# Kernel tuning notes

Measured on AMD Instinct MI355X. Metric: run time of the kernel, lower is better.

## Reference

```python
import jax, jax.numpy as jnp
import numpy as np

NUM_HEADS = 8
DIM_HEAD = 48
SCALE = DIM_HEAD ** -0.5


def setup_inputs() -> dict:
    key = jax.random.key(0)
    k1, k2, k3 = jax.random.split(key, 3)
    B, N, D = 4, 2048, 384
    inner = NUM_HEADS * DIM_HEAD  # 384
    x = jax.random.normal(k1, (B, N, D), dtype=jnp.float32)
    # store weights in [in, out] layout (equivalent to torch Linear W.T)
    Wqkv = jax.random.normal(k2, (D, 3 * inner), dtype=jnp.float32) * (D ** -0.5)
    Wproj = jax.random.normal(k3, (inner, D), dtype=jnp.float32) * (inner ** -0.5)
    bproj = jnp.zeros((D,), dtype=jnp.float32)
    return {"x": x, "Wqkv": Wqkv, "Wproj": Wproj, "bproj": bproj}


def reference(x, Wqkv, Wproj, bproj):
    B, N, D = x.shape
    h, dh = NUM_HEADS, DIM_HEAD
    C = h * dh
    # fused QKV projection (qkv_bias=False)
    qkv = (x @ Wqkv).reshape(B, N, 3, h, dh)
    q = qkv[:, :, 0].transpose(0, 2, 1, 3)  # [B, h, N, dh]
    k = qkv[:, :, 1].transpose(0, 2, 1, 3)
    v = qkv[:, :, 2].transpose(0, 2, 1, 3)
    # naive attention: materialize [B, h, N, N] scores
    sim = jnp.einsum("bhqd,bhkd->bhqk", q, k) * SCALE
    attn = jax.nn.softmax(sim, axis=-1)
    out = jnp.einsum("bhqk,bhkd->bhqd", attn, v)  # [B, h, N, dh]
    out = out.transpose(0, 2, 1, 3).reshape(B, N, C)
    return out @ Wproj + bproj
```

## Files before the change

kernel.cpp:

```cpp
#include <hip/hip_runtime.h>
#include <hip/hip_bf16.h>


typedef _Float16 f16x8 __attribute__((ext_vector_type(8)));
typedef _Float16 f16x4 __attribute__((ext_vector_type(4)));
typedef _Float16 f16x2 __attribute__((ext_vector_type(2)));
typedef float    f32x4 __attribute__((ext_vector_type(4)));
typedef float    f32x16 __attribute__((ext_vector_type(16)));

#define QSCL 0.20822035963448658f

static __device__ __forceinline__ f16x2 cvt_pk_f16(float a, float b) {
    return __builtin_bit_cast(f16x2, __builtin_amdgcn_cvt_pkrtz(a, b));
}

__global__ __launch_bounds__(256) void prep(const float4* __restrict__ x,
                                            const float* __restrict__ wq,
                                            const float* __restrict__ wp,
                                            f16x4* __restrict__ xh4,
                                            _Float16* __restrict__ wqt,
                                            _Float16* __restrict__ wpt)
{
    __shared__ _Float16 t[64][65];
    const int blk = blockIdx.x, tid = threadIdx.x;
    if (blk < 144) {
        const float* src; _Float16* dst; int Nn, k0, n0;
        if (blk < 108) {
            src = wq; dst = wqt; Nn = 1152;
            k0 = (blk % 6) * 64; n0 = (blk / 6) * 64;
        } else {
            const int b2 = blk - 108;
            src = wp; dst = wpt; Nn = 384;
            k0 = (b2 % 6) * 64; n0 = (b2 / 6) * 64;
        }
        #pragma unroll
        for (int i = 0; i < 16; i++) {
            const int id = tid + i * 256;
            const int k = id >> 6, n = id & 63;
            t[k][n] = (_Float16)src[(size_t)(k0 + k) * Nn + n0 + n];
        }
        __syncthreads();
        #pragma unroll
        for (int i = 0; i < 16; i++) {
            const int id = tid + i * 256;
            const int n = id >> 6, k = id & 63;
            dst[(size_t)(n0 + n) * 384 + k0 + k] = t[k][n];
        }
    } else {
        const int base = (blk - 144) * 3072;
        #pragma unroll
        for (int r = 0; r < 12; r++) {
            const int j = base + r * 256 + tid;
            const float4 tt = x[j];
            f16x4 hh;
            hh[0] = (_Float16)tt.x; hh[1] = (_Float16)tt.y;
            hh[2] = (_Float16)tt.z; hh[3] = (_Float16)tt.w;
            xh4[j] = hh;
        }
    }
}

union QkvSmem {
    struct { _Float16 As[2][128][40]; _Float16 Bs[2][128][40]; } g;
    _Float16 Ts[128][136];
    _Float16 Ts2[128][136];
};

__global__ __launch_bounds__(256) void qkv_f16(const _Float16* __restrict__ A,
                                               const _Float16* __restrict__ Bt,
                                               _Float16* __restrict__ qh,
                                               _Float16* __restrict__ kh,
                                               _Float16* __restrict__ vt)
{
    __shared__ QkvSmem sm;
    const int tid = threadIdx.x;
    const int w = tid >> 6, lane = tid & 63, cl = lane & 15, quad = lane >> 4;
    const int bm = blockIdx.x, bn = blockIdx.y;

    f32x4 acc[2][8];
    const f32x4 z4 = {0.f, 0.f, 0.f, 0.f};
    #pragma unroll
    for (int mi = 0; mi < 2; mi++)
        #pragma unroll
        for (int t = 0; t < 8; t++) acc[mi][t] = z4;

    const int ar = tid >> 2, ac = (tid & 3) * 8;
    const _Float16* Ag = A  + (size_t)(bm * 128 + ar) * 384 + ac;
    const _Float16* Bg = Bt + (size_t)(bn * 128 + ar) * 384 + ac;

    f16x8 pa[2], pb[2];
    #pragma unroll
    for (int j = 0; j < 2; j++) {
        pa[j] = *(const f16x8*)(Ag + (size_t)(64 * j) * 384);
        pb[j] = *(const f16x8*)(Bg + (size_t)(64 * j) * 384);
    }
    #pragma unroll
    for (int j = 0; j < 2; j++) {
        *(f16x8*)&sm.g.As[0][ar + 64 * j][ac] = pa[j];
        *(f16x8*)&sm.g.Bs[0][ar + 64 * j][ac] = pb[j];
    }
    #pragma unroll
    for (int j = 0; j < 2; j++) {
        pa[j] = *(const f16x8*)(Ag + (size_t)(64 * j) * 384 + 32);
        pb[j] = *(const f16x8*)(Bg + (size_t)(64 * j) * 384 + 32);
    }
    __syncthreads();

    for (int it = 0; it < 12; ++it) {
        if (it < 11) {
            #pragma unroll
            for (int j = 0; j < 2; j++) {
                *(f16x8*)&sm.g.As[(it + 1) & 1][ar + 64 * j][ac] = pa[j];
                *(f16x8*)&sm.g.Bs[(it + 1) & 1][ar + 64 * j][ac] = pb[j];
            }
            if (it < 10) {
                const int off = (it + 2) * 32;
                #pragma unroll
                for (int j = 0; j < 2; j++) {
                    pa[j] = *(const f16x8*)(Ag + (size_t)(64 * j) * 384 + off);
                    pb[j] = *(const f16x8*)(Bg + (size_t)(64 * j) * 384 + off);
                }
            }
        }
        f16x8 bf[8];
        #pragma unroll
        for (int t = 0; t < 8; t++)
            bf[t] = *(const f16x8*)&sm.g.Bs[it & 1][t * 16 + cl][quad * 8];
        #pragma unroll
        for (int mi = 0; mi < 2; mi++) {
            const f16x8 af = *(const f16x8*)&sm.g.As[it & 1][w * 32 + mi * 16 + cl][quad * 8];
            #pragma unroll
            for (int t = 0; t < 8; t++)
                acc[mi][t] = __builtin_amdgcn_mfma_f32_16x16x32_f16(af, bf[t], acc[mi][t], 0, 0, 0);
        }
        __syncthreads();
    }

    const int s = (bn * 128) / 384;
    const int b  = (bm * 128) >> 11;
    const int n0 = (bm * 128) & 2047;
    if (s == 2) {
        const int qp = ((quad & 1) << 1) | (quad >> 1);
        #pragma unroll
        for (int t = 0; t < 8; t++)
            #pragma unroll
            for (int mi = 0; mi < 2; mi++)
                #pragma unroll
                for (int r = 0; r < 4; r++)
                    sm.Ts[t * 16 + cl][w * 32 + mi * 16 + qp * 4 + r] =
                        (_Float16)acc[mi][t][r];
        __syncthreads();
        const int colbase = bn * 128 - 768;
        #pragma unroll
        for (int i = 0; i < 8; i++) {
            const int c = i * 256 + tid;
            const int col = c >> 4, nc = c & 15;
            const int gcol = colbase + col;
            const int head = gcol / 48, d = gcol - head * 48;
            const int bh = b * 8 + head;
            *(f16x8*)&vt[(size_t)(bh * 48 + d) * 2048 + n0 + nc * 8] =
                *(const f16x8*)&sm.Ts[col][nc * 8];
        }
    } else {
        const float scl = (s == 0) ? QSCL : 1.0f;
        #pragma unroll
        for (int t = 0; t < 8; t++)
            #pragma unroll
            for (int mi = 0; mi < 2; mi++)
                #pragma unroll
                for (int r = 0; r < 4; r++)
                    sm.Ts2[w * 32 + mi * 16 + quad * 4 + r][t * 16 + cl] =
                        (_Float16)(acc[mi][t][r] * scl);
        __syncthreads();
        _Float16* dst = (s == 0) ? qh : kh;
        const int colbase = bn * 128 - s * 384;
        #pragma unroll
        for (int i = 0; i < 8; i++) {
            const int c = i * 256 + tid;
            const int row = c >> 4, ch = c & 15;
            const int gcol = colbase + ch * 8;
            const int head = gcol / 48, d = gcol - head * 48;
            const int bh = b * 8 + head;
            *(f16x8*)&dst[(size_t)(bh * 2048 + n0 + row) * 48 + d] =
                *(const f16x8*)&sm.Ts2[row][ch * 8];
        }
    }
}

#define KS_S 56
#define VS_S 72

union AttnSmem {
    struct {
        _Float16 Ks[2][2][64][KS_S];
        _Float16 Vts[2][2][64][VS_S];
    } a;
    struct {
        float    Of[128][52];
        float    lv[128];
        _Float16 Ot[128][58];
    } e;
};

__global__ __launch_bounds__(512) void attn_f16(const _Float16* __restrict__ qh,
                                                const _Float16* __restrict__ kh,
                                                const _Float16* __restrict__ vt,
                                                _Float16* __restrict__ ab)
{
    __shared__ AttnSmem sm;
    const int tid = threadIdx.x;
    const int w = tid >> 6, lane = tid & 63, ln = lane & 31, h = lane >> 5;
    const int g = w >> 2, wg = w & 3;
    const int tid2 = tid & 255;
    const int bh = blockIdx.x, qt = blockIdx.y;

    for (int i = tid; i < 2 * 2 * 16 * VS_S; i += 512) {
        const int gi = i / (2 * 16 * VS_S);
        const int j  = i - gi * (2 * 16 * VS_S);
        const int bi = j / (16 * VS_S);
        const int j2 = j - bi * (16 * VS_S);
        const int r = 48 + j2 / VS_S, c = j2 % VS_S;
        sm.a.Vts[gi][bi][r][c] = (r == 48) ? (_Float16)1.0f : (_Float16)0.0f;
    }

    f16x8 qf[3];
    {
        const _Float16* qp = qh + (size_t)(bh * 2048 + qt * 128 + wg * 32 + ln) * 48 + 8 * h;
        qf[0] = *(const f16x8*)qp;
        qf[1] = *(const f16x8*)(qp + 16);
        qf[2] = *(const f16x8*)(qp + 32);
    }

    f32x16 o0, o1;
    #pragma unroll
    for (int r = 0; r < 16; r++) { o0[r] = 0.f; o1[r] = 0.f; }

    const _Float16* kbase = kh + (size_t)bh * 2048 * 48 + (size_t)g * 1024 * 48;
    const _Float16* vbase = vt + (size_t)bh * 48 * 2048 + g * 1024;

    const int kr0 = tid2 / 6,        kc0 = (tid2 % 6) * 8;
    const int kid1 = tid2 + 256;
    const int kr1 = kid1 / 6,        kc1 = (kid1 % 6) * 8;
    const int vr0 = tid2 >> 3,       vc0 = (tid2 & 7) * 8;
    const int vr1 = vr0 + 32;
    const _Float16* ks0 = kbase + (size_t)kr0 * 48 + kc0;
    const _Float16* ks1 = kbase + (size_t)kr1 * 48 + kc1;
    const _Float16* vs0 = vbase + (size_t)vr0 * 2048 + vc0;
    const _Float16* vs1 = vbase + (size_t)vr1 * 2048 + vc0;

    f16x8 rk0 = *(const f16x8*)ks0;
    f16x8 rv0 = *(const f16x8*)vs0;
    f16x8 rk1, rv1;
    if (tid2 < 128) { rk1 = *(const f16x8*)ks1; rv1 = *(const f16x8*)vs1; }

    {
        _Float16 (*Ksb)[KS_S] = sm.a.Ks[g][0];
        _Float16 (*Vtb)[VS_S] = sm.a.Vts[g][0];
        *(f16x8*)&Ksb[kr0][kc0] = rk0;
        *(f16x8*)&Vtb[vr0][vc0] = rv0;
        if (tid2 < 128) {
            *(f16x8*)&Ksb[kr1][kc1] = rk1;
            *(f16x8*)&Vtb[vr1][vc0] = rv1;
        }
        rk0 = *(const f16x8*)(ks0 + (size_t)64 * 48);
        rv0 = *(const f16x8*)(vs0 + 64);
        if (tid2 < 128) {
            rk1 = *(const f16x8*)(ks1 + (size_t)64 * 48);
            rv1 = *(const f16x8*)(vs1 + 64);
        }
        __syncthreads();
    }

    for (int t = 0; t < 16; ++t) {
        if (t < 15) {
            _Float16 (*Ksn)[KS_S] = sm.a.Ks[g][(t + 1) & 1];
            _Float16 (*Vtn)[VS_S] = sm.a.Vts[g][(t + 1) & 1];
            *(f16x8*)&Ksn[kr0][kc0] = rk0;
            *(f16x8*)&Vtn[vr0][vc0] = rv0;
            if (tid2 < 128) {
                *(f16x8*)&Ksn[kr1][kc1] = rk1;
                *(f16x8*)&Vtn[vr1][vc0] = rv1;
            }
            if (t < 14) {
                const int off = (t + 2) * 64;
                rk0 = *(const f16x8*)(ks0 + (size_t)off * 48);
                rv0 = *(const f16x8*)(vs0 + off);
                if (tid2 < 128) {
                    rk1 = *(const f16x8*)(ks1 + (size_t)off * 48);
                    rv1 = *(const f16x8*)(vs1 + off);
                }
            }
        }

        _Float16 (*Ksb)[KS_S] = sm.a.Ks[g][t & 1];
        _Float16 (*Vtb)[VS_S] = sm.a.Vts[g][t & 1];

        f32x16 s0, s1;
        #pragma unroll
        for (int r = 0; r < 16; r++) { s0[r] = 0.f; s1[r] = 0.f; }
        __builtin_amdgcn_s_setprio(1);
        #pragma unroll
        for (int i = 0; i < 3; i++) {
            const f16x8 ka0 = *(const f16x8*)&Ksb[ln][16 * i + 8 * h];
            s0 = __builtin_amdgcn_mfma_f32_32x32x16_f16(ka0, qf[i], s0, 0, 0, 0);
            const f16x8 ka1 = *(const f16x8*)&Ksb[32 + ln][16 * i + 8 * h];
            s1 = __builtin_amdgcn_mfma_f32_32x32x16_f16(ka1, qf[i], s1, 0, 0, 0);
        }
        __builtin_amdgcn_s_setprio(0);

        f16x8 pbf[4];
        f16x2* pp = (f16x2*)pbf;
        #pragma unroll
        for (int m = 0; m < 4; m++) {
            pp[m]      = cvt_pk_f16(
                __builtin_amdgcn_exp2f(s0[2 * m]),     __builtin_amdgcn_exp2f(s0[2 * m + 1]));
            pp[4 + m]  = cvt_pk_f16(
                __builtin_amdgcn_exp2f(s0[8 + 2 * m]), __builtin_amdgcn_exp2f(s0[9 + 2 * m]));
            pp[8 + m]  = cvt_pk_f16(
                __builtin_amdgcn_exp2f(s1[2 * m]),     __builtin_amdgcn_exp2f(s1[2 * m + 1]));
            pp[12 + m] = cvt_pk_f16(
                __builtin_amdgcn_exp2f(s1[8 + 2 * m]), __builtin_amdgcn_exp2f(s1[9 + 2 * m]));
        }

        __builtin_amdgcn_s_setprio(1);
        #pragma unroll
        for (int c = 0; c < 4; c++) {
            const f16x8 av0 = *(const f16x8*)&Vtb[ln][16 * c + 8 * h];
            o0 = __builtin_amdgcn_mfma_f32_32x32x16_f16(av0, pbf[c], o0, 0, 0, 0);
            const f16x8 av1 = *(const f16x8*)&Vtb[32 + ln][16 * c + 8 * h];
            o1 = __builtin_amdgcn_mfma_f32_32x32x16_f16(av1, pbf[c], o1, 0, 0, 0);
        }
        __builtin_amdgcn_s_setprio(0);

        __syncthreads();
    }

    const float lown = __shfl(o1[8], ln);

    const int row = wg * 32 + ln;
    if (g == 1) {
        #pragma unroll
        for (int q4 = 0; q4 < 4; q4++) {
            f32x4 tq = { o0[4 * q4], o0[4 * q4 + 1], o0[4 * q4 + 2], o0[4 * q4 + 3] };
            *(f32x4*)&sm.e.Of[row][8 * q4 + 4 * h] = tq;
        }
        #pragma unroll
        for (int q4 = 0; q4 < 2; q4++) {
            f32x4 tq = { o1[4 * q4], o1[4 * q4 + 1], o1[4 * q4 + 2], o1[4 * q4 + 3] };
            *(f32x4*)&sm.e.Of[row][32 + 8 * q4 + 4 * h] = tq;
        }
        if (h == 0) sm.e.lv[row] = o1[8];
    }
    __syncthreads();
    if (g == 0) {
        #pragma unroll
        for (int q4 = 0; q4 < 4; q4++) {
            const f32x4 tq = *(const f32x4*)&sm.e.Of[row][8 * q4 + 4 * h];
            o0[4 * q4] += tq[0]; o0[4 * q4 + 1] += tq[1];
            o0[4 * q4 + 2] += tq[2]; o0[4 * q4 + 3] += tq[3];
        }
        #pragma unroll
        for (int q4 = 0; q4 < 2; q4++) {
            const f32x4 tq = *(const f32x4*)&sm.e.Of[row][32 + 8 * q4 + 4 * h];
            o1[4 * q4] += tq[0]; o1[4 * q4 + 1] += tq[1];
            o1[4 * q4 + 2] += tq[2]; o1[4 * q4 + 3] += tq[3];
        }
        const float inv = 1.f / (lown + sm.e.lv[row]);
        #pragma unroll
        for (int r = 0; r < 16; r++)
            sm.e.Ot[row][(r & 3) + 8 * (r >> 2) + 4 * h] = (_Float16)(o0[r] * inv);
        #pragma unroll
        for (int r = 0; r < 8; r++)
            sm.e.Ot[row][32 + (r & 3) + 8 * (r >> 2) + 4 * h] = (_Float16)(o1[r] * inv);
    }
    __syncthreads();
    if (g == 0) {
        const int b = bh >> 3, hd = bh & 7;
        #pragma unroll
        for (int i = 0; i < 3; i++) {
            const int c2 = i * 256 + tid;
            const int rw = c2 / 6, ch = c2 % 6;
            const int q = qt * 128 + rw;
            *(f16x8*)&ab[(size_t)(b * 2048 + q) * 384 + hd * 48 + ch * 8] =
                *(const f16x8*)&sm.e.Ot[rw][ch * 8];
        }
    }
}

__global__ __launch_bounds__(256) void proj_f16(const _Float16* __restrict__ A,
                                                const _Float16* __restrict__ Bt,
                                                const float* __restrict__ bias,
                                                float* __restrict__ out)
{
    __shared__ _Float16 As[2][64][40];
    __shared__ _Float16 Bs[2][64][40];
    const int tid = threadIdx.x;
    const int w = tid >> 6, lane = tid & 63, cl = lane & 15, quad = lane >> 4;
    const int bm = blockIdx.x, bn = blockIdx.y;

    f32x4 acc[4];
    const f32x4 z4 = {0.f, 0.f, 0.f, 0.f};
    #pragma unroll
    for (int t = 0; t < 4; t++) acc[t] = z4;

    const int ar = tid >> 2, ac = (tid & 3) * 8;
    const _Float16* Ag = A  + (size_t)(bm * 64 + ar) * 384 + ac;
    const _Float16* Bg = Bt + (size_t)(bn * 64 + ar) * 384 + ac;

    f16x8 pa = *(const f16x8*)Ag;
    f16x8 pb = *(const f16x8*)Bg;
    *(f16x8*)&As[0][ar][ac] = pa;
    *(f16x8*)&Bs[0][ar][ac] = pb;
    pa = *(const f16x8*)(Ag + 32);
    pb = *(const f16x8*)(Bg + 32);
    __syncthreads();

    for (int it = 0; it < 12; ++it) {
        if (it < 11) {
            *(f16x8*)&As[(it + 1) & 1][ar][ac] = pa;
            *(f16x8*)&Bs[(it + 1) & 1][ar][ac] = pb;
            if (it < 10) {
                const int off = (it + 2) * 32;
                pa = *(const f16x8*)(Ag + off);
                pb = *(const f16x8*)(Bg + off);
            }
        }
        const f16x8 af = *(const f16x8*)&As[it & 1][w * 16 + cl][quad * 8];
        #pragma unroll
        for (int t = 0; t < 4; t++) {
            const f16x8 bf = *(const f16x8*)&Bs[it & 1][t * 16 + cl][quad * 8];
            acc[t] = __builtin_amdgcn_mfma_f32_16x16x32_f16(af, bf, acc[t], 0, 0, 0);
        }
        __syncthreads();
    }

    #pragma unroll
    for (int t = 0; t < 4; t++) {
        const int col = bn * 64 + t * 16 + cl;
        const float bv = bias[col];
        #pragma unroll
        for (int r = 0; r < 4; r++) {
            const int row = bm * 64 + w * 16 + quad * 4 + r;
            out[(size_t)row * 384 + col] = acc[t][r] + bv;
        }
    }
}

extern "C" void kernel_launch(void* const* d_in, const int* in_sizes, int n_in,
                              void* d_out, int out_size, void* d_ws, size_t ws_size,
                              hipStream_t stream) {
    const float* x     = (const float*)d_in[0];
    const float* Wqkv  = (const float*)d_in[1];
    const float* Wproj = (const float*)d_in[2];
    const float* bproj = (const float*)d_in[3];
    float* out = (float*)d_out;

    char* ws = (char*)d_ws;
    _Float16* xh     = (_Float16*)(ws + 0);
    _Float16* wqkvt  = (_Float16*)(ws + 6291456);
    _Float16* wprojt = (_Float16*)(ws + 7176192);
    _Float16* qh     = (_Float16*)(ws + 7471104);
    _Float16* kh     = (_Float16*)(ws + 13762560);
    _Float16* vt     = (_Float16*)(ws + 20054016);
    _Float16* ab     = (_Float16*)(ws + 26345472);

    prep<<<400, 256, 0, stream>>>((const float4*)x, Wqkv, Wproj,
                                  (f16x4*)xh, wqkvt, wprojt);
    qkv_f16<<<dim3(64, 9), 256, 0, stream>>>(xh, wqkvt, qh, kh, vt);
    attn_f16<<<dim3(32, 16), 512, 0, stream>>>(qh, kh, vt, ab);
    proj_f16<<<dim3(128, 6), 256, 0, stream>>>(ab, wprojt, bproj, out);
}
```

Measured before the change: 128.7 us.

## Fuse x fp32-to-fp16 conversion into QKV GEMM loads and remap block order

Removes the separate x conversion pass from the prep kernel: the QKV GEMM now loads fp32 x directly and converts it to fp16 while staging it into shared memory. This drops a 6 MB fp16 intermediate write and its re-read, and shrinks prep to the weight transposes only. Both GEMMs also switch to a 1D grid with a permuted block-to-tile mapping, likely to spread tiles across XCDs and improve L2 locality. In exchange, the QKV kernel reads twice the bytes for A per tile and does the conversion redundantly across the 9 column blocks.

New measurement: 129.9 us. Within noise of the previous version (+1.0%).

```diff
diff --git a/kernel.cpp b/kernel.cpp
--- a/kernel.cpp
+++ b/kernel.cpp
@@ -13,50 +13,41 @@
 static __device__ __forceinline__ f16x2 cvt_pk_f16(float a, float b) {
     return __builtin_bit_cast(f16x2, __builtin_amdgcn_cvt_pkrtz(a, b));
 }
-
-__global__ __launch_bounds__(256) void prep(const float4* __restrict__ x,
-                                            const float* __restrict__ wq,
+static __device__ __forceinline__ f16x8 cvt_f16x8(float4 a, float4 b) {
+    f16x8 r; f16x2* rp = (f16x2*)&r;
+    rp[0] = cvt_pk_f16(a.x, a.y); rp[1] = cvt_pk_f16(a.z, a.w);
+    rp[2] = cvt_pk_f16(b.x, b.y); rp[3] = cvt_pk_f16(b.z, b.w);
+    return r;
+}
+
+__global__ __launch_bounds__(256) void prep(const float* __restrict__ wq,
                                             const float* __restrict__ wp,
-                                            f16x4* __restrict__ xh4,
                                             _Float16* __restrict__ wqt,
                                             _Float16* __restrict__ wpt)
 {
     __shared__ _Float16 t[64][65];
     const int blk = blockIdx.x, tid = threadIdx.x;
-    if (blk < 144) {
-        const float* src; _Float16* dst; int Nn, k0, n0;
-        if (blk < 108) {
-            src = wq; dst = wqt; Nn = 1152;
-            k0 = (blk % 6) * 64; n0 = (blk / 6) * 64;
-        } else {
-            const int b2 = blk - 108;
-            src = wp; dst = wpt; Nn = 384;
-            k0 = (b2 % 6) * 64; n0 = (b2 / 6) * 64;
-        }
-        #pragma unroll
-        for (int i = 0; i < 16; i++) {
-            const int id = tid + i * 256;
-            const int k = id >> 6, n = id & 63;
-            t[k][n] = (_Float16)src[(size_t)(k0 + k) * Nn + n0 + n];
-        }
-        __syncthreads();
-        #pragma unroll
-        for (int i = 0; i < 16; i++) {
-            const int id = tid + i * 256;
-            const int n = id >> 6, k = id & 63;
-            dst[(size_t)(n0 + n) * 384 + k0 + k] = t[k][n];
-        }
+    const float* src; _Float16* dst; int Nn, k0, n0;
+    if (blk < 108) {
+        src = wq; dst = wqt; Nn = 1152;
+        k0 = (blk % 6) * 64; n0 = (blk / 6) * 64;
     } else {
-        const int base = (blk - 144) * 3072;
-        #pragma unroll
-        for (int r = 0; r < 12; r++) {
-            const int j = base + r * 256 + tid;
-            const float4 tt = x[j];
-            f16x4 hh;
-            hh[0] = (_Float16)tt.x; hh[1] = (_Float16)tt.y;
-            hh[2] = (_Float16)tt.z; hh[3] = (_Float16)tt.w;
-            xh4[j] = hh;
-        }
+        const int b2 = blk - 108;
+        src = wp; dst = wpt; Nn = 384;
+        k0 = (b2 % 6) * 64; n0 = (b2 / 6) * 64;
+    }
+    #pragma unroll
+    for (int i = 0; i < 16; i++) {
+        const int id = tid + i * 256;
+        const int k = id >> 6, n = id & 63;
+        t[k][n] = (_Float16)src[(size_t)(k0 + k) * Nn + n0 + n];
+    }
+    __syncthreads();
+    #pragma unroll
+    for (int i = 0; i < 16; i++) {
+        const int id = tid + i * 256;
+        const int n = id >> 6, k = id & 63;
+        dst[(size_t)(n0 + n) * 384 + k0 + k] = t[k][n];
     }
 }
 
@@ -66,7 +57,7 @@
     _Float16 Ts2[128][136];
 };
 
-__global__ __launch_bounds__(256) void qkv_f16(const _Float16* __restrict__ A,
+__global__ __launch_bounds__(256) void qkv_f16(const float* __restrict__ X,
                                                const _Float16* __restrict__ Bt,
                                                _Float16* __restrict__ qh,
                                                _Float16* __restrict__ kh,
@@ -75,7 +66,9 @@
     __shared__ QkvSmem sm;
     const int tid = threadIdx.x;
     const int w = tid >> 6, lane = tid & 63, cl = lane & 15, quad = lane >> 4;
-    const int bm = blockIdx.x, bn = blockIdx.y;
+    const int p = blockIdx.x;
+    const int l = (p & 7) * 72 + (p >> 3);
+    const int bm = l / 9, bn = l - 9 * bm;
 
     f32x4 acc[2][8];
     const f32x4 z4 = {0.f, 0.f, 0.f, 0.f};
@@ -85,24 +78,26 @@
         for (int t = 0; t < 8; t++) acc[mi][t] = z4;
 
     const int ar = tid >> 2, ac = (tid & 3) * 8;
-    const _Float16* Ag = A  + (size_t)(bm * 128 + ar) * 384 + ac;
+    const float*    Ag = X  + (size_t)(bm * 128 + ar) * 384 + ac;
     const _Float16* Bg = Bt + (size_t)(bn * 128 + ar) * 384 + ac;
 
-    f16x8 pa[2], pb[2];
+    float4 pa[2][2]; f16x8 pb[2];
     #pragma unroll
     for (int j = 0; j < 2; j++) {
-        pa[j] = *(const f16x8*)(Ag + (size_t)(64 * j) * 384);
-        pb[j] = *(const f16x8*)(Bg + (size_t)(64 * j) * 384);
+        pa[j][0] = *(const float4*)(Ag + (size_t)(64 * j) * 384);
+        pa[j][1] = *(const float4*)(Ag + (size_t)(64 * j) * 384 + 4);
+        pb[j]    = *(const f16x8*)(Bg + (size_t)(64 * j) * 384);
     }
     #pragma unroll
     for (int j = 0; j < 2; j++) {
-        *(f16x8*)&sm.g.As[0][ar + 64 * j][ac] = pa[j];
+        *(f16x8*)&sm.g.As[0][ar + 64 * j][ac] = cvt_f16x8(pa[j][0], pa[j][1]);
         *(f16x8*)&sm.g.Bs[0][ar + 64 * j][ac] = pb[j];
     }
     #pragma unroll
     for (int j = 0; j < 2; j++) {
-        pa[j] = *(const f16x8*)(Ag + (size_t)(64 * j) * 384 + 32);
-        pb[j] = *(const f16x8*)(Bg + (size_t)(64 * j) * 384 + 32);
+        pa[j][0] = *(const float4*)(Ag + (size_t)(64 * j) * 384 + 32);
+        pa[j][1] = *(const float4*)(Ag + (size_t)(64 * j) * 384 + 36);
+        pb[j]    = *(const f16x8*)(Bg + (size_t)(64 * j) * 384 + 32);
     }
     __syncthreads();
 
@@ -110,15 +105,16 @@
         if (it < 11) {
             #pragma unroll
             for (int j = 0; j < 2; j++) {
-                *(f16x8*)&sm.g.As[(it + 1) & 1][ar + 64 * j][ac] = pa[j];
+                *(f16x8*)&sm.g.As[(it + 1) & 1][ar + 64 * j][ac] = cvt_f16x8(pa[j][0], pa[j][1]);
                 *(f16x8*)&sm.g.Bs[(it + 1) & 1][ar + 64 * j][ac] = pb[j];
             }
             if (it < 10) {
                 const int off = (it + 2) * 32;
                 #pragma unroll
                 for (int j = 0; j < 2; j++) {
-                    pa[j] = *(const f16x8*)(Ag + (size_t)(64 * j) * 384 + off);
-                    pb[j] = *(const f16x8*)(Bg + (size_t)(64 * j) * 384 + off);
+                    pa[j][0] = *(const float4*)(Ag + (size_t)(64 * j) * 384 + off);
+                    pa[j][1] = *(const float4*)(Ag + (size_t)(64 * j) * 384 + off + 4);
+                    pb[j]    = *(const f16x8*)(Bg + (size_t)(64 * j) * 384 + off);
                 }
             }
         }
@@ -396,7 +392,9 @@
     __shared__ _Float16 Bs[2][64][40];
     const int tid = threadIdx.x;
     const int w = tid >> 6, lane = tid & 63, cl = lane & 15, quad = lane >> 4;
-    const int bm = blockIdx.x, bn = blockIdx.y;
+    const int p = blockIdx.x;
+    const int l = (p & 7) * 96 + (p >> 3);
+    const int bm = l / 6, bn = l - 6 * bm;
 
     f32x4 acc[4];
     const f32x4 z4 = {0.f, 0.f, 0.f, 0.f};
@@ -456,17 +454,15 @@
     float* out = (float*)d_out;
 
     char* ws = (char*)d_ws;
-    _Float16* xh     = (_Float16*)(ws + 0);
-    _Float16* wqkvt  = (_Float16*)(ws + 6291456);
-    _Float16* wprojt = (_Float16*)(ws + 7176192);
-    _Float16* qh     = (_Float16*)(ws + 7471104);
-    _Float16* kh     = (_Float16*)(ws + 13762560);
-    _Float16* vt     = (_Float16*)(ws + 20054016);
-    _Float16* ab     = (_Float16*)(ws + 26345472);
-
-    prep<<<400, 256, 0, stream>>>((const float4*)x, Wqkv, Wproj,
-                                  (f16x4*)xh, wqkvt, wprojt);
-    qkv_f16<<<dim3(64, 9), 256, 0, stream>>>(xh, wqkvt, qh, kh, vt);
+    _Float16* wqkvt  = (_Float16*)(ws + 0);
+    _Float16* wprojt = (_Float16*)(ws + 884736);
+    _Float16* qh     = (_Float16*)(ws + 1179648);
+    _Float16* kh     = (_Float16*)(ws + 7471104);
+    _Float16* vt     = (_Float16*)(ws + 13762560);
+    _Float16* ab     = (_Float16*)(ws + 20054016);
+
+    prep<<<144, 256, 0, stream>>>(Wqkv, Wproj, wqkvt, wprojt);
+    qkv_f16<<<576, 256, 0, stream>>>(x, wqkvt, qh, kh, vt);
     attn_f16<<<dim3(32, 16), 512, 0, stream>>>(qh, kh, vt, ab);
-    proj_f16<<<dim3(128, 6), 256, 0, stream>>>(ab, wprojt, bproj, out);
-}
+    proj_f16<<<768, 256, 0, stream>>>(ab, wprojt, bproj, out);
+}
```
